# Kernel optimization log

Hardware: AMD Instinct MI355X
Metric: run time of the kernel (lower is better)

Reference implementation:

```python
import jax, jax.numpy as jnp
import numpy as np

N = 100000       # nodes
E0 = 1600000     # edges without self loops
E = E0 + N       # with self loops appended (attr 0), matching add_self_loops
DIN = 128        # input_dim
HID = 64         # nb_hidden_gnn (per-head out_channels)
HEADS = 4
EMB = 128
L = 3            # nb_layer
NEG_SLOPE = 0.2
BN_EPS = 1e-5


def setup_inputs() -> dict:
    key = jax.random.key(0)
    ks = jax.random.split(key, 12)
    # edges with no self loops; self loops (i,i) appended with edge_attr 0
    row = jax.random.randint(ks[0], (E0,), 0, N)
    off = jax.random.randint(ks[1], (E0,), 1, N)
    col = (row + off) % N
    loops = jnp.arange(N, dtype=row.dtype)
    edge_index = jnp.stack([jnp.concatenate([row, loops]),
                            jnp.concatenate([col, loops])])
    edge_attr = jnp.concatenate([jax.random.normal(ks[2], (E0, 1), jnp.float32),
                                 jnp.zeros((N, 1), jnp.float32)])
    x = jax.random.normal(ks[3], (N, DIN), jnp.float32)
    HC = HEADS * HID
    linN0 = jax.random.normal(ks[4], (DIN, HC)) * HC ** -0.5
    linN_rest = jax.random.normal(ks[5], (L - 1, HID, HC)) * HC ** -0.5
    linE_all = jax.random.normal(ks[6], (L, 1, HEADS)) * HEADS ** -0.5  # nb_edge_attr=1
    att_all = jax.random.normal(ks[7], (L, HEADS, 2 * HID + 1)) * (2 * HID + 1) ** -0.5
    bias_all = jnp.zeros((L, HID))  # concat=False -> bias [out_channels]
    bn_gamma = jnp.ones((L - 1, HID))
    bn_beta = jnp.zeros((L - 1, HID))
    W = jax.random.normal(ks[8], (HID, EMB)) * HID ** -0.5
    b = jnp.zeros((EMB,))
    return {"x": x, "edge_index": edge_index, "edge_attr": edge_attr,
            "linN0": linN0, "linN_rest": linN_rest, "linE_all": linE_all,
            "att_all": att_all, "bias_all": bias_all,
            "bn_gamma": bn_gamma, "bn_beta": bn_beta, "W": W, "b": b}


def _gcn_layer(x, row, col, edge_attr, linN, linE, att, bias, bn):
    n = x.shape[0]
    if bn is not None:
        gamma, beta = bn
        mu = x.mean(axis=0)
        var = x.var(axis=0)
        x = (x - mu) * jax.lax.rsqrt(var + BN_EPS) * gamma + beta
    h = (x @ linN).reshape(n, HEADS, HID)                 # [N,H,C]
    e = (edge_attr @ linE)                                # [E,H] (nb_edge_attr=1)
    att_i = att[:, :HID]                                  # [H,C]
    att_j = att[:, HID:2 * HID]                           # [H,C]
    att_e = att[:, 2 * HID:]                              # [H,1]
    # per-node partial scores avoid gathering full features twice
    s_i = jnp.einsum('nhc,hc->nh', h, att_i)
    s_j = jnp.einsum('nhc,hc->nh', h, att_j)
    logits = s_i[row] + s_j[col] + e * att_e[:, 0]        # [E,H]
    logits = jax.nn.leaky_relu(logits, NEG_SLOPE)
    # segment softmax over destination nodes (edge_index[1])
    m = jax.ops.segment_max(logits, col, num_segments=n)
    p = jnp.exp(logits - m[col])
    denom = jax.ops.segment_sum(p, col, num_segments=n)
    alpha = p / (denom[col] + 1e-16)
    # message: alpha * x[source], scatter-add to destination
    msg = alpha[:, :, None] * h[row]                      # [E,H,C]
    out = jax.ops.segment_sum(msg, col, num_segments=n)   # [N,H,C]
    out = out.mean(axis=1) + bias + h.mean(axis=1)        # concat=False, res=True
    return jax.nn.relu(out)


def reference(x, edge_index, edge_attr, linN0, linN_rest, linE_all, att_all,
              bias_all, bn_gamma, bn_beta, W, b):
    row, col = edge_index[0], edge_index[1]
    emb = x
    for l in range(L):
        linN = linN0 if l == 0 else linN_rest[l - 1]
        bn = None if l == 0 else (bn_gamma[l - 1], bn_beta[l - 1])
        emb = _gcn_layer(emb, row, col, edge_attr, linN, linE_all[l],
                         att_all[l], bias_all[l], bn)
    return emb @ W + b
```

## Files before the change

kernel.cpp:

```cpp
#include <hip/hip_runtime.h>
#include <math.h>

#define NN 100000
#define E0E 1600000
#define EE (E0E + NN)
#define NEG 0.2f
#define BNEPS 1e-5f
#define LOG2E 1.4426950408889634f

typedef float f4 __attribute__((ext_vector_type(4)));
typedef float f2 __attribute__((ext_vector_type(2)));
typedef short s8v __attribute__((ext_vector_type(8)));

__device__ __forceinline__ float wred_max(float v) {
#pragma unroll
  for (int m = 1; m < 64; m <<= 1) v = fmaxf(v, __shfl_xor(v, m, 64));
  return v;
}
__device__ __forceinline__ float wred_sum(float v) {
#pragma unroll
  for (int m = 1; m < 64; m <<= 1) v += __shfl_xor(v, m, 64);
  return v;
}
__device__ __forceinline__ float sel4(float a0, float a1, float a2, float a3, int hd) {
  return (hd & 2) ? ((hd & 1) ? a3 : a2) : ((hd & 1) ? a1 : a0);
}
__device__ __forceinline__ unsigned short f2bf(float x) {
  unsigned u = __float_as_uint(x);
  return (unsigned short)((u + 0x7fffu + ((u >> 16) & 1u)) >> 16);
}
__device__ __forceinline__ float bf2f(unsigned short s) {
  return __uint_as_float(((unsigned)s) << 16);
}

__global__ void k_zero_i32(int* p, int n) {
  int i = blockIdx.x * blockDim.x + threadIdx.x;
  if (i < n) p[i] = 0;
}
__global__ void k_zero_f64(double* p, int n) {
  int i = blockIdx.x * blockDim.x + threadIdx.x;
  if (i < n) p[i] = 0.0;
}
__global__ void k_count(const int* __restrict__ col, int* cnt, int e) {
  int i = blockIdx.x * blockDim.x + threadIdx.x;
  if (i < e) atomicAdd(&cnt[col[i]], 1);
}
#define SCAN_T 1024
__global__ void k_scan1(const int* __restrict__ cnt, int* partial, int n, int chunk) {
  int i = blockIdx.x * blockDim.x + threadIdx.x;
  int beg = i * chunk, end = min(n, beg + chunk);
  int s = 0;
  for (int j = beg; j < end; ++j) s += cnt[j];
  partial[i] = s;
}
__global__ void k_scan2(int* partial) {
  __shared__ int lds[SCAN_T];
  int t = threadIdx.x;
  int v = partial[t];
  lds[t] = v;
  __syncthreads();
  for (int off = 1; off < SCAN_T; off <<= 1) {
    int add = (t >= off) ? lds[t - off] : 0;
    __syncthreads();
    lds[t] += add;
    __syncthreads();
  }
  partial[t] = lds[t] - v;
}
__global__ void k_scan3(const int* __restrict__ cnt, const int* __restrict__ partial,
                        int* rowptr, int* cursor, int n, int chunk, int etot) {
  int i = blockIdx.x * blockDim.x + threadIdx.x;
  int beg = i * chunk, end = min(n, beg + chunk);
  int run = partial[i];
  for (int j = beg; j < end; ++j) {
    rowptr[j] = run;
    cursor[j] = run;
    run += cnt[j];
  }
  if (i == SCAN_T - 1) rowptr[n] = etot;
}
__global__ void k_scatter(const int* __restrict__ row, const int* __restrict__ col,
                          const float* __restrict__ ea, int* cursor, int2* csr, int e) {
  int i = blockIdx.x * blockDim.x + threadIdx.x;
  if (i < e) {
    int c = col[i];
    int p = atomicAdd(&cursor[c], 1);
    csr[p] = make_int2(row[i], __float_as_int(ea[i]));
  }
}

__global__ void k_bnstats(const float* __restrict__ x, double* sums, int n) {
  int f = threadIdx.x & 63;
  int rt = (blockIdx.x * blockDim.x + threadIdx.x) >> 6;
  int rstride = (gridDim.x * blockDim.x) >> 6;
  double s = 0.0, q = 0.0;
  for (int r = rt; r < n; r += rstride) {
    double v = (double)x[(size_t)r * 64 + f];
    s += v;
    q += v * v;
  }
  __shared__ double ls[256], lq[256];
  ls[threadIdx.x] = s;
  lq[threadIdx.x] = q;
  __syncthreads();
  if (threadIdx.x < 64) {
    s = ls[threadIdx.x] + ls[threadIdx.x + 64] + ls[threadIdx.x + 128] + ls[threadIdx.x + 192];
    q = lq[threadIdx.x] + lq[threadIdx.x + 64] + lq[threadIdx.x + 128] + lq[threadIdx.x + 192];
    atomicAdd(&sums[f], s);
    atomicAdd(&sums[64 + f], q);
  }
}
__global__ void k_bnfinal(const double* __restrict__ sums, const float* __restrict__ gamma,
                          const float* __restrict__ beta, float* AB, int n) {
  int f = threadIdx.x;
  if (f < 64) {
    double mean = sums[f] / n;
    double var = sums[64 + f] / n - mean * mean;
    float A = gamma[f] * rsqrtf((float)var + BNEPS);
    AB[f] = A;
    AB[64 + f] = beta[f] - (float)mean * A;
  }
}

__global__ void k_prepw(const float* __restrict__ W, const float* __restrict__ AB,
                        const float* __restrict__ bin, unsigned short* __restrict__ Wt,
                        float* __restrict__ cvec, int K, int N, int mode) {
  int n = threadIdx.x;
  if (n >= N) return;
  float c = (mode == 2) ? bin[n] : 0.f;
  for (int k = 0; k < K; ++k) {
    float w = W[k * N + n];
    float a = 1.f, b = 0.f;
    if (mode == 1) { a = AB[k]; b = AB[64 + k]; }
    Wt[n * K + k] = f2bf(a * w);
    c = fmaf(b, w, c);
  }
  cvec[n] = c;
}

template <int K, int CT, bool ATT, bool OB>
__global__ __launch_bounds__(256, 2) void k_gemm(const float* __restrict__ x,
                                                 const unsigned short* __restrict__ Wt,
                                                 const float* __restrict__ cvec,
                                                 const float* __restrict__ att,
                                                 void* __restrict__ houtv,
                                                 float* __restrict__ s_i,
                                                 float* __restrict__ s_j, int n,
                                                 int ntiles) {
  constexpr int KS = K / 32;
  constexpr int ROWB = 2 * K;
  constexpr int CPR = K / 8;
  constexpr int NCOL = 4 * CT * 16;
  __shared__ unsigned char xs[64 * ROWB];
  const int lane = threadIdx.x & 63;
  const int wv = threadIdx.x >> 6;
  const int l15 = lane & 15;
  const int lq = lane >> 4;
  const int colbase = wv * CT * 16;

  s8v wfr[CT][KS];
#pragma unroll
  for (int ct = 0; ct < CT; ++ct)
#pragma unroll
    for (int ks = 0; ks < KS; ++ks)
      wfr[ct][ks] = *(const s8v*)&Wt[(size_t)(colbase + ct * 16 + l15) * K + ks * 32 + lq * 8];
  float cb[CT][4];
#pragma unroll
  for (int ct = 0; ct < CT; ++ct)
#pragma unroll
    for (int r = 0; r < 4; ++r) cb[ct][r] = cvec[colbase + ct * 16 + lq * 4 + r];
  float ati[ATT ? CT : 1][4], atj[ATT ? CT : 1][4];
  if constexpr (ATT) {
    const float* ar = att + wv * 129;
#pragma unroll
    for (int ct = 0; ct < CT; ++ct)
#pragma unroll
      for (int r = 0; r < 4; ++r) {
        int cc = ct * 16 + lq * 4 + r;
        ati[ct][r] = ar[cc];
        atj[ct][r] = ar[64 + cc];
      }
  }

  for (int t = blockIdx.x; t < ntiles; t += gridDim.x) {
    const int row0 = t * 64;
    __syncthreads();
#pragma unroll
    for (int i = 0; i < (64 * CPR) / 256; ++i) {
      int c = threadIdx.x + i * 256;
      int row = c / CPR, kc = c % CPR;
      int rg = min(row0 + row, n - 1);
      const float* xp = x + (size_t)rg * K + kc * 8;
      f4 a0 = *(const f4*)xp;
      f4 a1 = *(const f4*)(xp + 4);
      union { s8v v; unsigned short u[8]; } pk;
      pk.u[0] = f2bf(a0[0]); pk.u[1] = f2bf(a0[1]); pk.u[2] = f2bf(a0[2]); pk.u[3] = f2bf(a0[3]);
      pk.u[4] = f2bf(a1[0]); pk.u[5] = f2bf(a1[1]); pk.u[6] = f2bf(a1[2]); pk.u[7] = f2bf(a1[3]);
      *(s8v*)&xs[row * ROWB + ((kc * 16) ^ ((row & 7) << 4))] = pk.v;
    }
    __syncthreads();
    f4 acc[4][CT];
#pragma unroll
    for (int rt = 0; rt < 4; ++rt)
#pragma unroll
      for (int ct = 0; ct < CT; ++ct) acc[rt][ct] = (f4)0.f;
#pragma unroll
    for (int ks = 0; ks < KS; ++ks) {
      s8v xf[4];
#pragma unroll
      for (int rt = 0; rt < 4; ++rt) {
        int row = rt * 16 + l15;
        int kb = ks * 64 + lq * 16;
        xf[rt] = *(const s8v*)&xs[row * ROWB + (kb ^ ((row & 7) << 4))];
      }
#pragma unroll
      for (int rt = 0; rt < 4; ++rt)
#pragma unroll
        for (int ct = 0; ct < CT; ++ct)
          acc[rt][ct] = __builtin_amdgcn_mfma_f32_16x16x32_bf16(wfr[ct][ks], xf[rt],
                                                                acc[rt][ct], 0, 0, 0);
    }
#pragma unroll
    for (int rt = 0; rt < 4; ++rt) {
      if (row0 + rt * 16 >= n) continue;
      const size_t xrow = (size_t)(row0 + rt * 16 + l15);
      float v[CT][4];
#pragma unroll
      for (int ct = 0; ct < CT; ++ct)
#pragma unroll
        for (int r = 0; r < 4; ++r) v[ct][r] = acc[rt][ct][r] + cb[ct][r];
      if constexpr (OB) {
        float* outp = (float*)houtv;
#pragma unroll
        for (int ct = 0; ct < CT; ++ct) {
          f4 o;
          o[0] = v[ct][0]; o[1] = v[ct][1]; o[2] = v[ct][2]; o[3] = v[ct][3];
          *(f4*)&outp[xrow * NCOL + colbase + ct * 16 + lq * 4] = o;
        }
      } else {
        unsigned short* hout = (unsigned short*)houtv;
#pragma unroll
        for (int ct = 0; ct < CT; ++ct) {
          ushort4 hb4;
          hb4.x = f2bf(v[ct][0]); hb4.y = f2bf(v[ct][1]);
          hb4.z = f2bf(v[ct][2]); hb4.w = f2bf(v[ct][3]);
          *(ushort4*)&hout[xrow * NCOL + colbase + ct * 16 + lq * 4] = hb4;
        }
      }
      if constexpr (ATT) {
        float pi = 0.f, pj = 0.f;
#pragma unroll
        for (int ct = 0; ct < CT; ++ct)
#pragma unroll
          for (int r = 0; r < 4; ++r) {
            pi = fmaf(v[ct][r], ati[ct][r], pi);
            pj = fmaf(v[ct][r], atj[ct][r], pj);
          }
        pi += __shfl_xor(pi, 16, 64); pi += __shfl_xor(pi, 32, 64);
        pj += __shfl_xor(pj, 16, 64); pj += __shfl_xor(pj, 32, 64);
        if (lane < 16) {
          s_i[xrow * 4 + wv] = pi;
          s_j[xrow * 4 + wv] = pj;
        }
      }
    }
  }
}

__global__ __launch_bounds__(256) void k_edge(const int* __restrict__ rowptr,
                                              const int2* __restrict__ csr,
                                              const float* __restrict__ s_i,
                                              const float* __restrict__ s_j,
                                              const unsigned short* __restrict__ hb,
                                              const float* __restrict__ linE,
                                              const float* __restrict__ att,
                                              const float* __restrict__ bias,
                                              float* __restrict__ xout, int n) {
  __shared__ float lp[4][64][4];
  __shared__ int lsrc[4][64];
  const int lane = threadIdx.x & 63;
  const int wid = threadIdx.x >> 6;
  int v = blockIdx.x * 4 + wid;
  if (v >= n) return;
  v = __builtin_amdgcn_readfirstlane(v);
  const int base = rowptr[v];
  const int deg = rowptr[v + 1] - base;

  const float coef0 = linE[0] * att[0 * 129 + 128];
  const float coef1 = linE[1] * att[1 * 129 + 128];
  const float coef2 = linE[2] * att[2 * 129 + 128];
  const float coef3 = linE[3] * att[3 * 129 + 128];
  const float sj0 = s_j[(size_t)v * 4 + 0];
  const float sj1 = s_j[(size_t)v * 4 + 1];
  const float sj2 = s_j[(size_t)v * 4 + 2];
  const float sj3 = s_j[(size_t)v * 4 + 3];

  auto edge_logits = [&](int i, int& src, float& g0, float& g1, float& g2, float& g3) {
    int2 pk = csr[i];
    src = pk.x;
    float ea = __int_as_float(pk.y);
    f4 siv = *(const f4*)&s_i[(size_t)src * 4];
    g0 = siv[0] + sj0 + ea * coef0; g0 = fmaxf(g0, g0 * NEG);
    g1 = siv[1] + sj1 + ea * coef1; g1 = fmaxf(g1, g1 * NEG);
    g2 = siv[2] + sj2 + ea * coef2; g2 = fmaxf(g2, g2 * NEG);
    g3 = siv[3] + sj3 + ea * coef3; g3 = fmaxf(g3, g3 * NEG);
  };

  const int hd = lane >> 4;
  float msel, rdsel;
  bool fast = (deg <= 64);
  if (fast) {
    float g0 = -INFINITY, g1 = -INFINITY, g2 = -INFINITY, g3 = -INFINITY;
    int src = 0;
    bool valid = lane < deg;
    if (valid) edge_logits(base + lane, src, g0, g1, g2, g3);
    float m0 = wred_max(g0), m1 = wred_max(g1), m2 = wred_max(g2), m3 = wred_max(g3);
    float p0 = valid ? exp2f((g0 - m0) * LOG2E) : 0.f;
    float p1 = valid ? exp2f((g1 - m1) * LOG2E) : 0.f;
    float p2 = valid ? exp2f((g2 - m2) * LOG2E) : 0.f;
    float p3 = valid ? exp2f((g3 - m3) * LOG2E) : 0.f;
    if (valid) {
      f4 pp; pp[0] = p0; pp[1] = p1; pp[2] = p2; pp[3] = p3;
      *(f4*)&lp[wid][lane][0] = pp;
      lsrc[wid][lane] = src;
    }
    float d0 = wred_sum(p0), d1 = wred_sum(p1), d2 = wred_sum(p2), d3 = wred_sum(p3);
    rdsel = 1.f / (sel4(d0, d1, d2, d3, hd) + 1e-16f);
    msel = 0.f;
  } else {
    float m0 = -INFINITY, m1 = -INFINITY, m2 = -INFINITY, m3 = -INFINITY;
    for (int c0 = 0; c0 < deg; c0 += 64) {
      int i = c0 + lane;
      if (i < deg) {
        int src; float g0, g1, g2, g3;
        edge_logits(base + i, src, g0, g1, g2, g3);
        m0 = fmaxf(m0, g0); m1 = fmaxf(m1, g1); m2 = fmaxf(m2, g2); m3 = fmaxf(m3, g3);
      }
    }
    m0 = wred_max(m0); m1 = wred_max(m1); m2 = wred_max(m2); m3 = wred_max(m3);
    float d0 = 0, d1 = 0, d2 = 0, d3 = 0;
    for (int c0 = 0; c0 < deg; c0 += 64) {
      int i = c0 + lane;
      if (i < deg) {
        int src; float g0, g1, g2, g3;
        edge_logits(base + i, src, g0, g1, g2, g3);
        d0 += exp2f((g0 - m0) * LOG2E);
        d1 += exp2f((g1 - m1) * LOG2E);
        d2 += exp2f((g2 - m2) * LOG2E);
        d3 += exp2f((g3 - m3) * LOG2E);
      }
    }
    d0 = wred_sum(d0); d1 = wred_sum(d1); d2 = wred_sum(d2); d3 = wred_sum(d3);
    msel = sel4(m0, m1, m2, m3, hd);
    rdsel = 1.f / (sel4(d0, d1, d2, d3, hd) + 1e-16f);
  }

  f4 acc;
  {
    ushort4 hr = *(const ushort4*)&hb[(size_t)v * 256 + lane * 4];
    acc[0] = bf2f(hr.x); acc[1] = bf2f(hr.y); acc[2] = bf2f(hr.z); acc[3] = bf2f(hr.w);
  }
  if (fast) {
    for (int e = 0; e < deg; ++e) {
      int src = lsrc[wid][e];
      float a = lp[wid][e][hd] * rdsel;
      ushort4 hr = *(const ushort4*)&hb[(size_t)src * 256 + lane * 4];
      acc[0] = fmaf(a, bf2f(hr.x), acc[0]);
      acc[1] = fmaf(a, bf2f(hr.y), acc[1]);
      acc[2] = fmaf(a, bf2f(hr.z), acc[2]);
      acc[3] = fmaf(a, bf2f(hr.w), acc[3]);
    }
  } else {
    const float sjsel = sel4(sj0, sj1, sj2, sj3, hd);
    const float cfsel = sel4(coef0, coef1, coef2, coef3, hd);
    for (int e = base; e < base + deg; ++e) {
      int2 pk = csr[e];
      int src = pk.x;
      float ea = __int_as_float(pk.y);
      f4 siv = *(const f4*)&s_i[(size_t)src * 4];
      float lg = sel4(siv[0], siv[1], siv[2], siv[3], hd) + sjsel + ea * cfsel;
      lg = fmaxf(lg, lg * NEG);
      float a = exp2f((lg - msel) * LOG2E) * rdsel;
      ushort4 hr = *(const ushort4*)&hb[(size_t)src * 256 + lane * 4];
      acc[0] = fmaf(a, bf2f(hr.x), acc[0]);
      acc[1] = fmaf(a, bf2f(hr.y), acc[1]);
      acc[2] = fmaf(a, bf2f(hr.z), acc[2]);
      acc[3] = fmaf(a, bf2f(hr.w), acc[3]);
    }
  }
#pragma unroll
  for (int m = 16; m < 64; m <<= 1) {
    acc[0] += __shfl_xor(acc[0], m, 64);
    acc[1] += __shfl_xor(acc[1], m, 64);
    acc[2] += __shfl_xor(acc[2], m, 64);
    acc[3] += __shfl_xor(acc[3], m, 64);
  }
  if (lane < 16) {
    f4 bv = *(const f4*)&bias[lane * 4];
    f4 o;
#pragma unroll
    for (int c = 0; c < 4; ++c) o[c] = fmaxf(acc[c] * 0.25f + bv[c], 0.f);
    *(f4*)&xout[(size_t)v * 64 + lane * 4] = o;
  }
}

extern "C" void kernel_launch(void* const* d_in, const int* in_sizes, int n_in,
                              void* d_out, int out_size, void* d_ws, size_t ws_size,
                              hipStream_t stream) {
  const float* x_in = (const float*)d_in[0];
  const int* ei = (const int*)d_in[1];
  const float* eattr = (const float*)d_in[2];
  const float* linN0 = (const float*)d_in[3];
  const float* linNr = (const float*)d_in[4];
  const float* linE = (const float*)d_in[5];
  const float* attA = (const float*)d_in[6];
  const float* biasA = (const float*)d_in[7];
  const float* bng = (const float*)d_in[8];
  const float* bnb = (const float*)d_in[9];
  const float* W = (const float*)d_in[10];
  const float* bb = (const float*)d_in[11];
  float* out = (float*)d_out;

  const int* row = ei;
  const int* col = ei + EE;

  char* ws = (char*)d_ws;
  size_t o = 0;
  auto alloc = [&](size_t bytes) {
    void* p = ws + o;
    o += (bytes + 255) & ~(size_t)255;
    return p;
  };
  int* cnt = (int*)alloc((size_t)NN * 4);
  int* cursor = (int*)alloc((size_t)NN * 4);
  int* rowptr = (int*)alloc((size_t)(NN + 1) * 4);
  int* partial = (int*)alloc((size_t)SCAN_T * 4);
  int2* csr = (int2*)alloc((size_t)EE * 8);
  unsigned short* h = (unsigned short*)alloc((size_t)NN * 256 * 2);
  float* si = (float*)alloc((size_t)NN * 4 * 4);
  float* sj = (float*)alloc((size_t)NN * 4 * 4);
  float* xa = (float*)alloc((size_t)NN * 64 * 4);
  float* xb = (float*)alloc((size_t)NN * 64 * 4);
  double* bnsum = (double*)alloc(256 * 8);
  float* AB = (float*)alloc(128 * 4);
  unsigned short* Wt = (unsigned short*)alloc((size_t)256 * 128 * 2);
  float* cvec = (float*)alloc(256 * 4);
  if (o > ws_size) return;

  const int chunk = (NN + SCAN_T - 1) / SCAN_T;
  const int NTILES = (NN + 63) / 64;
  const int GG = 521;

  k_zero_i32<<<(NN + 255) / 256, 256, 0, stream>>>(cnt, NN);
  k_zero_f64<<<1, 256, 0, stream>>>(bnsum, 256);
  k_count<<<(EE + 255) / 256, 256, 0, stream>>>(col, cnt, EE);
  k_scan1<<<4, 256, 0, stream>>>(cnt, partial, NN, chunk);
  k_scan2<<<1, SCAN_T, 0, stream>>>(partial);
  k_scan3<<<4, 256, 0, stream>>>(cnt, partial, rowptr, cursor, NN, chunk, EE);
  k_scatter<<<(EE + 255) / 256, 256, 0, stream>>>(row, col, eattr, cursor, csr, EE);

  k_prepw<<<1, 256, 0, stream>>>(linN0, nullptr, nullptr, Wt, cvec, 128, 256, 0);
  k_gemm<128, 4, true, false><<<GG, 256, 0, stream>>>(x_in, Wt, cvec, attA + 0, h, si, sj,
                                                      NN, NTILES);
  k_edge<<<NN / 4, 256, 0, stream>>>(rowptr, csr, si, sj, h, linE + 0, attA + 0, biasA + 0, xa, NN);

  k_bnstats<<<256, 256, 0, stream>>>(xa, bnsum, NN);
  k_bnfinal<<<1, 64, 0, stream>>>(bnsum, bng + 0, bnb + 0, AB, NN);
  k_prepw<<<1, 256, 0, stream>>>(linNr, AB, nullptr, Wt, cvec, 64, 256, 1);
  k_gemm<64, 4, true, false><<<GG, 256, 0, stream>>>(xa, Wt, cvec, attA + 516, h, si, sj,
                                                     NN, NTILES);
  k_edge<<<NN / 4, 256, 0, stream>>>(rowptr, csr, si, sj, h, linE + 4, attA + 516, biasA + 64, xb, NN);

  k_bnstats<<<256, 256, 0, stream>>>(xb, bnsum + 128, NN);
  k_bnfinal<<<1, 64, 0, stream>>>(bnsum + 128, bng + 64, bnb + 64, AB, NN);
  k_prepw<<<1, 256, 0, stream>>>(linNr + 64 * 256, AB, nullptr, Wt, cvec, 64, 256, 1);
  k_gemm<64, 4, true, false><<<GG, 256, 0, stream>>>(xb, Wt, cvec, attA + 2 * 516, h, si, sj,
                                                     NN, NTILES);
  k_edge<<<NN / 4, 256, 0, stream>>>(rowptr, csr, si, sj, h, linE + 8, attA + 2 * 516, biasA + 128, xa, NN);

  k_prepw<<<1, 256, 0, stream>>>(W, nullptr, bb, Wt, cvec, 64, 128, 2);
  k_gemm<64, 2, false, true><<<GG, 256, 0, stream>>>(xa, Wt, cvec, nullptr, out, nullptr,
                                                     nullptr, NN, NTILES);
}
```

Before: 940.1 us.

## Fuse batchnorm statistics into edge kernel and persistent-loop edge aggregation

The edge-aggregation kernel becomes a grid-stride persistent loop over nodes. It accumulates per-feature sums and sums of squares of its output, then reduces them per block and adds them atomically into the batchnorm buffer. This removes the separate stats pass that re-read the activations, and the finalize step moves into the weight-prep kernel. The zeroing kernels are merged into one, the fast-path gather is unrolled by four for more loads in flight, and the gemm grid now uses one block per tile instead of a fixed count. Statistics are now accumulated in float per thread before the double atomics, which slightly changes precision.

```diff
diff --git a/kernel.cpp b/kernel.cpp
--- a/kernel.cpp
+++ b/kernel.cpp
@@ -33,13 +33,10 @@
   return __uint_as_float(((unsigned)s) << 16);
 }
 
-__global__ void k_zero_i32(int* p, int n) {
+__global__ void k_init(int* cnt, double* bnsum, int n) {
   int i = blockIdx.x * blockDim.x + threadIdx.x;
-  if (i < n) p[i] = 0;
-}
-__global__ void k_zero_f64(double* p, int n) {
-  int i = blockIdx.x * blockDim.x + threadIdx.x;
-  if (i < n) p[i] = 0.0;
+  if (i < n) cnt[i] = 0;
+  if (i < 256) bnsum[i] = 0.0;
 }
 __global__ void k_count(const int* __restrict__ col, int* cnt, int e) {
   int i = blockIdx.x * blockDim.x + threadIdx.x;
@@ -89,53 +86,32 @@
   }
 }
 
-__global__ void k_bnstats(const float* __restrict__ x, double* sums, int n) {
-  int f = threadIdx.x & 63;
-  int rt = (blockIdx.x * blockDim.x + threadIdx.x) >> 6;
-  int rstride = (gridDim.x * blockDim.x) >> 6;
-  double s = 0.0, q = 0.0;
-  for (int r = rt; r < n; r += rstride) {
-    double v = (double)x[(size_t)r * 64 + f];
-    s += v;
-    q += v * v;
-  }
-  __shared__ double ls[256], lq[256];
-  ls[threadIdx.x] = s;
-  lq[threadIdx.x] = q;
-  __syncthreads();
-  if (threadIdx.x < 64) {
-    s = ls[threadIdx.x] + ls[threadIdx.x + 64] + ls[threadIdx.x + 128] + ls[threadIdx.x + 192];
-    q = lq[threadIdx.x] + lq[threadIdx.x + 64] + lq[threadIdx.x + 128] + lq[threadIdx.x + 192];
-    atomicAdd(&sums[f], s);
-    atomicAdd(&sums[64 + f], q);
-  }
-}
-__global__ void k_bnfinal(const double* __restrict__ sums, const float* __restrict__ gamma,
-                          const float* __restrict__ beta, float* AB, int n) {
-  int f = threadIdx.x;
-  if (f < 64) {
-    double mean = sums[f] / n;
-    double var = sums[64 + f] / n - mean * mean;
-    float A = gamma[f] * rsqrtf((float)var + BNEPS);
-    AB[f] = A;
-    AB[64 + f] = beta[f] - (float)mean * A;
-  }
-}
-
-__global__ void k_prepw(const float* __restrict__ W, const float* __restrict__ AB,
+__global__ void k_prepw(const float* __restrict__ W, const double* __restrict__ bnsum,
+                        const float* __restrict__ gamma, const float* __restrict__ beta,
                         const float* __restrict__ bin, unsigned short* __restrict__ Wt,
                         float* __restrict__ cvec, int K, int N, int mode) {
-  int n = threadIdx.x;
-  if (n >= N) return;
-  float c = (mode == 2) ? bin[n] : 0.f;
+  __shared__ float ABl[128];
+  int t = threadIdx.x;
+  if (mode == 1) {
+    if (t < 64) {
+      double mean = bnsum[t] / NN;
+      double var = bnsum[64 + t] / NN - mean * mean;
+      float A = gamma[t] * rsqrtf((float)var + BNEPS);
+      ABl[t] = A;
+      ABl[64 + t] = beta[t] - (float)mean * A;
+    }
+    __syncthreads();
+  }
+  if (t >= N) return;
+  float c = (mode == 2) ? bin[t] : 0.f;
   for (int k = 0; k < K; ++k) {
-    float w = W[k * N + n];
+    float w = W[k * N + t];
     float a = 1.f, b = 0.f;
-    if (mode == 1) { a = AB[k]; b = AB[64 + k]; }
-    Wt[n * K + k] = f2bf(a * w);
+    if (mode == 1) { a = ABl[k]; b = ABl[64 + k]; }
+    Wt[t * K + k] = f2bf(a * w);
     c = fmaf(b, w, c);
   }
-  cvec[n] = c;
+  cvec[t] = c;
 }
 
 template <int K, int CT, bool ATT, bool OB>
@@ -267,6 +243,7 @@
   }
 }
 
+template <bool BNS>
 __global__ __launch_bounds__(256) void k_edge(const int* __restrict__ rowptr,
                                               const int2* __restrict__ csr,
                                               const float* __restrict__ s_i,
@@ -275,132 +252,184 @@
                                               const float* __restrict__ linE,
                                               const float* __restrict__ att,
                                               const float* __restrict__ bias,
-                                              float* __restrict__ xout, int n) {
+                                              float* __restrict__ xout,
+                                              double* __restrict__ bnsum, int n) {
   __shared__ float lp[4][64][4];
   __shared__ int lsrc[4][64];
+  __shared__ float bS[4][64], bQ[4][64];
   const int lane = threadIdx.x & 63;
   const int wid = threadIdx.x >> 6;
-  int v = blockIdx.x * 4 + wid;
-  if (v >= n) return;
-  v = __builtin_amdgcn_readfirstlane(v);
-  const int base = rowptr[v];
-  const int deg = rowptr[v + 1] - base;
+  const int hd = lane >> 4;
 
   const float coef0 = linE[0] * att[0 * 129 + 128];
   const float coef1 = linE[1] * att[1 * 129 + 128];
   const float coef2 = linE[2] * att[2 * 129 + 128];
   const float coef3 = linE[3] * att[3 * 129 + 128];
-  const float sj0 = s_j[(size_t)v * 4 + 0];
-  const float sj1 = s_j[(size_t)v * 4 + 1];
-  const float sj2 = s_j[(size_t)v * 4 + 2];
-  const float sj3 = s_j[(size_t)v * 4 + 3];
-
-  auto edge_logits = [&](int i, int& src, float& g0, float& g1, float& g2, float& g3) {
-    int2 pk = csr[i];
-    src = pk.x;
-    float ea = __int_as_float(pk.y);
-    f4 siv = *(const f4*)&s_i[(size_t)src * 4];
-    g0 = siv[0] + sj0 + ea * coef0; g0 = fmaxf(g0, g0 * NEG);
-    g1 = siv[1] + sj1 + ea * coef1; g1 = fmaxf(g1, g1 * NEG);
-    g2 = siv[2] + sj2 + ea * coef2; g2 = fmaxf(g2, g2 * NEG);
-    g3 = siv[3] + sj3 + ea * coef3; g3 = fmaxf(g3, g3 * NEG);
-  };
-
-  const int hd = lane >> 4;
-  float msel, rdsel;
-  bool fast = (deg <= 64);
-  if (fast) {
-    float g0 = -INFINITY, g1 = -INFINITY, g2 = -INFINITY, g3 = -INFINITY;
-    int src = 0;
-    bool valid = lane < deg;
-    if (valid) edge_logits(base + lane, src, g0, g1, g2, g3);
-    float m0 = wred_max(g0), m1 = wred_max(g1), m2 = wred_max(g2), m3 = wred_max(g3);
-    float p0 = valid ? exp2f((g0 - m0) * LOG2E) : 0.f;
-    float p1 = valid ? exp2f((g1 - m1) * LOG2E) : 0.f;
-    float p2 = valid ? exp2f((g2 - m2) * LOG2E) : 0.f;
-    float p3 = valid ? exp2f((g3 - m3) * LOG2E) : 0.f;
-    if (valid) {
-      f4 pp; pp[0] = p0; pp[1] = p1; pp[2] = p2; pp[3] = p3;
-      *(f4*)&lp[wid][lane][0] = pp;
-      lsrc[wid][lane] = src;
-    }
-    float d0 = wred_sum(p0), d1 = wred_sum(p1), d2 = wred_sum(p2), d3 = wred_sum(p3);
-    rdsel = 1.f / (sel4(d0, d1, d2, d3, hd) + 1e-16f);
-    msel = 0.f;
-  } else {
-    float m0 = -INFINITY, m1 = -INFINITY, m2 = -INFINITY, m3 = -INFINITY;
-    for (int c0 = 0; c0 < deg; c0 += 64) {
-      int i = c0 + lane;
-      if (i < deg) {
-        int src; float g0, g1, g2, g3;
-        edge_logits(base + i, src, g0, g1, g2, g3);
-        m0 = fmaxf(m0, g0); m1 = fmaxf(m1, g1); m2 = fmaxf(m2, g2); m3 = fmaxf(m3, g3);
-      }
-    }
-    m0 = wred_max(m0); m1 = wred_max(m1); m2 = wred_max(m2); m3 = wred_max(m3);
-    float d0 = 0, d1 = 0, d2 = 0, d3 = 0;
-    for (int c0 = 0; c0 < deg; c0 += 64) {
-      int i = c0 + lane;
-      if (i < deg) {
-        int src; float g0, g1, g2, g3;
-        edge_logits(base + i, src, g0, g1, g2, g3);
-        d0 += exp2f((g0 - m0) * LOG2E);
-        d1 += exp2f((g1 - m1) * LOG2E);
-        d2 += exp2f((g2 - m2) * LOG2E);
-        d3 += exp2f((g3 - m3) * LOG2E);
-      }
-    }
-    d0 = wred_sum(d0); d1 = wred_sum(d1); d2 = wred_sum(d2); d3 = wred_sum(d3);
-    msel = sel4(m0, m1, m2, m3, hd);
-    rdsel = 1.f / (sel4(d0, d1, d2, d3, hd) + 1e-16f);
-  }
-
-  f4 acc;
-  {
-    ushort4 hr = *(const ushort4*)&hb[(size_t)v * 256 + lane * 4];
-    acc[0] = bf2f(hr.x); acc[1] = bf2f(hr.y); acc[2] = bf2f(hr.z); acc[3] = bf2f(hr.w);
-  }
-  if (fast) {
-    for (int e = 0; e < deg; ++e) {
-      int src = lsrc[wid][e];
-      float a = lp[wid][e][hd] * rdsel;
-      ushort4 hr = *(const ushort4*)&hb[(size_t)src * 256 + lane * 4];
-      acc[0] = fmaf(a, bf2f(hr.x), acc[0]);
-      acc[1] = fmaf(a, bf2f(hr.y), acc[1]);
-      acc[2] = fmaf(a, bf2f(hr.z), acc[2]);
-      acc[3] = fmaf(a, bf2f(hr.w), acc[3]);
-    }
-  } else {
-    const float sjsel = sel4(sj0, sj1, sj2, sj3, hd);
-    const float cfsel = sel4(coef0, coef1, coef2, coef3, hd);
-    for (int e = base; e < base + deg; ++e) {
-      int2 pk = csr[e];
-      int src = pk.x;
+  float accS[4] = {0.f, 0.f, 0.f, 0.f}, accQ[4] = {0.f, 0.f, 0.f, 0.f};
+
+  for (int v0 = blockIdx.x * 4 + wid; v0 < n; v0 += gridDim.x * 4) {
+    const int v = __builtin_amdgcn_readfirstlane(v0);
+    const int base = rowptr[v];
+    const int deg = rowptr[v + 1] - base;
+    const float sj0 = s_j[(size_t)v * 4 + 0];
+    const float sj1 = s_j[(size_t)v * 4 + 1];
+    const float sj2 = s_j[(size_t)v * 4 + 2];
+    const float sj3 = s_j[(size_t)v * 4 + 3];
+
+    f4 accI;
+    {
+      ushort4 hr = *(const ushort4*)&hb[(size_t)v * 256 + lane * 4];
+      accI[0] = bf2f(hr.x); accI[1] = bf2f(hr.y); accI[2] = bf2f(hr.z); accI[3] = bf2f(hr.w);
+    }
+
+    auto edge_logits = [&](int i, int& src, float& g0, float& g1, float& g2, float& g3) {
+      int2 pk = csr[i];
+      src = pk.x;
       float ea = __int_as_float(pk.y);
       f4 siv = *(const f4*)&s_i[(size_t)src * 4];
-      float lg = sel4(siv[0], siv[1], siv[2], siv[3], hd) + sjsel + ea * cfsel;
-      lg = fmaxf(lg, lg * NEG);
-      float a = exp2f((lg - msel) * LOG2E) * rdsel;
-      ushort4 hr = *(const ushort4*)&hb[(size_t)src * 256 + lane * 4];
-      acc[0] = fmaf(a, bf2f(hr.x), acc[0]);
-      acc[1] = fmaf(a, bf2f(hr.y), acc[1]);
-      acc[2] = fmaf(a, bf2f(hr.z), acc[2]);
-      acc[3] = fmaf(a, bf2f(hr.w), acc[3]);
-    }
-  }
-#pragma unroll
-  for (int m = 16; m < 64; m <<= 1) {
-    acc[0] += __shfl_xor(acc[0], m, 64);
-    acc[1] += __shfl_xor(acc[1], m, 64);
-    acc[2] += __shfl_xor(acc[2], m, 64);
-    acc[3] += __shfl_xor(acc[3], m, 64);
-  }
-  if (lane < 16) {
-    f4 bv = *(const f4*)&bias[lane * 4];
-    f4 o;
-#pragma unroll
-    for (int c = 0; c < 4; ++c) o[c] = fmaxf(acc[c] * 0.25f + bv[c], 0.f);
-    *(f4*)&xout[(size_t)v * 64 + lane * 4] = o;
+      g0 = siv[0] + sj0 + ea * coef0; g0 = fmaxf(g0, g0 * NEG);
+      g1 = siv[1] + sj1 + ea * coef1; g1 = fmaxf(g1, g1 * NEG);
+      g2 = siv[2] + sj2 + ea * coef2; g2 = fmaxf(g2, g2 * NEG);
+      g3 = siv[3] + sj3 + ea * coef3; g3 = fmaxf(g3, g3 * NEG);
+    };
+
+    float rdsel;
+    f4 accE = {0.f, 0.f, 0.f, 0.f};
+    bool fast = (deg <= 64);
+    if (fast) {
+      float g0 = -INFINITY, g1 = -INFINITY, g2 = -INFINITY, g3 = -INFINITY;
+      int src = 0;
+      bool valid = lane < deg;
+      if (valid) edge_logits(base + lane, src, g0, g1, g2, g3);
+      float m0 = wred_max(g0), m1 = wred_max(g1), m2 = wred_max(g2), m3 = wred_max(g3);
+      float p0 = valid ? exp2f((g0 - m0) * LOG2E) : 0.f;
+      float p1 = valid ? exp2f((g1 - m1) * LOG2E) : 0.f;
+      float p2 = valid ? exp2f((g2 - m2) * LOG2E) : 0.f;
+      float p3 = valid ? exp2f((g3 - m3) * LOG2E) : 0.f;
+      if (valid) {
+        f4 pp; pp[0] = p0; pp[1] = p1; pp[2] = p2; pp[3] = p3;
+        *(f4*)&lp[wid][lane][0] = pp;
+        lsrc[wid][lane] = src;
+      }
+      float d0 = wred_sum(p0), d1 = wred_sum(p1), d2 = wred_sum(p2), d3 = wred_sum(p3);
+      rdsel = 1.f / (sel4(d0, d1, d2, d3, hd) + 1e-16f);
+      int e = 0;
+      for (; e + 4 <= deg; e += 4) {
+        int s0 = lsrc[wid][e + 0], s1 = lsrc[wid][e + 1];
+        int s2 = lsrc[wid][e + 2], s3 = lsrc[wid][e + 3];
+        float a0 = lp[wid][e + 0][hd], a1 = lp[wid][e + 1][hd];
+        float a2 = lp[wid][e + 2][hd], a3 = lp[wid][e + 3][hd];
+        ushort4 h0 = *(const ushort4*)&hb[(size_t)s0 * 256 + lane * 4];
+        ushort4 h1 = *(const ushort4*)&hb[(size_t)s1 * 256 + lane * 4];
+        ushort4 h2 = *(const ushort4*)&hb[(size_t)s2 * 256 + lane * 4];
+        ushort4 h3 = *(const ushort4*)&hb[(size_t)s3 * 256 + lane * 4];
+        accE[0] = fmaf(a0, bf2f(h0.x), accE[0]); accE[1] = fmaf(a0, bf2f(h0.y), accE[1]);
+        accE[2] = fmaf(a0, bf2f(h0.z), accE[2]); accE[3] = fmaf(a0, bf2f(h0.w), accE[3]);
+        accE[0] = fmaf(a1, bf2f(h1.x), accE[0]); accE[1] = fmaf(a1, bf2f(h1.y), accE[1]);
+        accE[2] = fmaf(a1, bf2f(h1.z), accE[2]); accE[3] = fmaf(a1, bf2f(h1.w), accE[3]);
+        accE[0] = fmaf(a2, bf2f(h2.x), accE[0]); accE[1] = fmaf(a2, bf2f(h2.y), accE[1]);
+        accE[2] = fmaf(a2, bf2f(h2.z), accE[2]); accE[3] = fmaf(a2, bf2f(h2.w), accE[3]);
+        accE[0] = fmaf(a3, bf2f(h3.x), accE[0]); accE[1] = fmaf(a3, bf2f(h3.y), accE[1]);
+        accE[2] = fmaf(a3, bf2f(h3.z), accE[2]); accE[3] = fmaf(a3, bf2f(h3.w), accE[3]);
+      }
+      for (; e < deg; ++e) {
+        int s0 = lsrc[wid][e];
+        float a0 = lp[wid][e][hd];
+        ushort4 h0 = *(const ushort4*)&hb[(size_t)s0 * 256 + lane * 4];
+        accE[0] = fmaf(a0, bf2f(h0.x), accE[0]); accE[1] = fmaf(a0, bf2f(h0.y), accE[1]);
+        accE[2] = fmaf(a0, bf2f(h0.z), accE[2]); accE[3] = fmaf(a0, bf2f(h0.w), accE[3]);
+      }
+    } else {
+      float m0 = -INFINITY, m1 = -INFINITY, m2 = -INFINITY, m3 = -INFINITY;
+      for (int c0 = 0; c0 < deg; c0 += 64) {
+        int i = c0 + lane;
+        if (i < deg) {
+          int src; float g0, g1, g2, g3;
+          edge_logits(base + i, src, g0, g1, g2, g3);
+          m0 = fmaxf(m0, g0); m1 = fmaxf(m1, g1); m2 = fmaxf(m2, g2); m3 = fmaxf(m3, g3);
+        }
+      }
+      m0 = wred_max(m0); m1 = wred_max(m1); m2 = wred_max(m2); m3 = wred_max(m3);
+      float d0 = 0, d1 = 0, d2 = 0, d3 = 0;
+      for (int c0 = 0; c0 < deg; c0 += 64) {
+        int i = c0 + lane;
+        if (i < deg) {
+          int src; float g0, g1, g2, g3;
+          edge_logits(base + i, src, g0, g1, g2, g3);
+          d0 += exp2f((g0 - m0) * LOG2E);
+          d1 += exp2f((g1 - m1) * LOG2E);
+          d2 += exp2f((g2 - m2) * LOG2E);
+          d3 += exp2f((g3 - m3) * LOG2E);
+        }
+      }
+      d0 = wred_sum(d0); d1 = wred_sum(d1); d2 = wred_sum(d2); d3 = wred_sum(d3);
+      float msel = sel4(m0, m1, m2, m3, hd);
+      rdsel = 1.f / (sel4(d0, d1, d2, d3, hd) + 1e-16f);
+      const float sjsel = sel4(sj0, sj1, sj2, sj3, hd);
+      const float cfsel = sel4(coef0, coef1, coef2, coef3, hd);
+      for (int e = base; e < base + deg; ++e) {
+        int2 pk = csr[e];
+        int src = pk.x;
+        float ea = __int_as_float(pk.y);
+        f4 siv = *(const f4*)&s_i[(size_t)src * 4];
+        float lg = sel4(siv[0], siv[1], siv[2], siv[3], hd) + sjsel + ea * cfsel;
+        lg = fmaxf(lg, lg * NEG);
+        float a = exp2f((lg - msel) * LOG2E);
+        ushort4 hr = *(const ushort4*)&hb[(size_t)src * 256 + lane * 4];
+        accE[0] = fmaf(a, bf2f(hr.x), accE[0]);
+        accE[1] = fmaf(a, bf2f(hr.y), accE[1]);
+        accE[2] = fmaf(a, bf2f(hr.z), accE[2]);
+        accE[3] = fmaf(a, bf2f(hr.w), accE[3]);
+      }
+    }
+    f4 acc;
+#pragma unroll
+    for (int c = 0; c < 4; ++c) acc[c] = fmaf(rdsel, accE[c], accI[c]);
+#pragma unroll
+    for (int m = 16; m < 64; m <<= 1) {
+      acc[0] += __shfl_xor(acc[0], m, 64);
+      acc[1] += __shfl_xor(acc[1], m, 64);
+      acc[2] += __shfl_xor(acc[2], m, 64);
+      acc[3] += __shfl_xor(acc[3], m, 64);
+    }
+    if (lane < 16) {
+      f4 bv = *(const f4*)&bias[lane * 4];
+      f4 o;
+#pragma unroll
+      for (int c = 0; c < 4; ++c) o[c] = fmaxf(acc[c] * 0.25f + bv[c], 0.f);
+      *(f4*)&xout[(size_t)v * 64 + lane * 4] = o;
+      if constexpr (BNS) {
+#pragma unroll
+        for (int c = 0; c < 4; ++c) {
+          accS[c] += o[c];
+          accQ[c] += o[c] * o[c];
+        }
+      }
+    }
+  }
+
+  if constexpr (BNS) {
+    if (lane < 16) {
+#pragma unroll
+      for (int c = 0; c < 4; ++c) {
+        bS[wid][lane * 4 + c] = accS[c];
+        bQ[wid][lane * 4 + c] = accQ[c];
+      }
+    }
+    __syncthreads();
+    int t = threadIdx.x;
+    if (t < 64) {
+      float s = 0.f;
+#pragma unroll
+      for (int w = 0; w < 4; ++w) s += bS[w][t];
+      atomicAdd(&bnsum[t], (double)s);
+    } else if (t < 128) {
+      int f = t - 64;
+      float q = 0.f;
+#pragma unroll
+      for (int w = 0; w < 4; ++w) q += bQ[w][f];
+      atomicAdd(&bnsum[64 + f], (double)q);
+    }
   }
 }
 
@@ -442,43 +471,41 @@
   float* xa = (float*)alloc((size_t)NN * 64 * 4);
   float* xb = (float*)alloc((size_t)NN * 64 * 4);
   double* bnsum = (double*)alloc(256 * 8);
-  float* AB = (float*)alloc(128 * 4);
   unsigned short* Wt = (unsigned short*)alloc((size_t)256 * 128 * 2);
   float* cvec = (float*)alloc(256 * 4);
   if (o > ws_size) return;
 
   const int chunk = (NN + SCAN_T - 1) / SCAN_T;
   const int NTILES = (NN + 63) / 64;
-  const int GG = 521;
-
-  k_zero_i32<<<(NN + 255) / 256, 256, 0, stream>>>(cnt, NN);
-  k_zero_f64<<<1, 256, 0, stream>>>(bnsum, 256);
+  const int EG = 2048;
+
+  k_init<<<(NN + 255) / 256, 256, 0, stream>>>(cnt, bnsum, NN);
   k_count<<<(EE + 255) / 256, 256, 0, stream>>>(col, cnt, EE);
   k_scan1<<<4, 256, 0, stream>>>(cnt, partial, NN, chunk);
   k_scan2<<<1, SCAN_T, 0, stream>>>(partial);
   k_scan3<<<4, 256, 0, stream>>>(cnt, partial, rowptr, cursor, NN, chunk, EE);
   k_scatter<<<(EE + 255) / 256, 256, 0, stream>>>(row, col, eattr, cursor, csr, EE);
 
-  k_prepw<<<1, 256, 0, stream>>>(linN0, nullptr, nullptr, Wt, cvec, 128, 256, 0);
-  k_gemm<128, 4, true, false><<<GG, 256, 0, stream>>>(x_in, Wt, cvec, attA + 0, h, si, sj,
-                                                      NN, NTILES);
-  k_edge<<<NN / 4, 256, 0, stream>>>(rowptr, csr, si, sj, h, linE + 0, attA + 0, biasA + 0, xa, NN);
-
-  k_bnstats<<<256, 256, 0, stream>>>(xa, bnsum, NN);
-  k_bnfinal<<<1, 64, 0, stream>>>(bnsum, bng + 0, bnb + 0, AB, NN);
-  k_prepw<<<1, 256, 0, stream>>>(linNr, AB, nullptr, Wt, cvec, 64, 256, 1);
-  k_gemm<64, 4, true, false><<<GG, 256, 0, stream>>>(xa, Wt, cvec, attA + 516, h, si, sj,
-                                                     NN, NTILES);
-  k_edge<<<NN / 4, 256, 0, stream>>>(rowptr, csr, si, sj, h, linE + 4, attA + 516, biasA + 64, xb, NN);
-
-  k_bnstats<<<256, 256, 0, stream>>>(xb, bnsum + 128, NN);
-  k_bnfinal<<<1, 64, 0, stream>>>(bnsum + 128, bng + 64, bnb + 64, AB, NN);
-  k_prepw<<<1, 256, 0, stream>>>(linNr + 64 * 256, AB, nullptr, Wt, cvec, 64, 256, 1);
-  k_gemm<64, 4, true, false><<<GG, 256, 0, stream>>>(xb, Wt, cvec, attA + 2 * 516, h, si, sj,
-                                                     NN, NTILES);
-  k_edge<<<NN / 4, 256, 0, stream>>>(rowptr, csr, si, sj, h, linE + 8, attA + 2 * 516, biasA + 128, xa, NN);
-
-  k_prepw<<<1, 256, 0, stream>>>(W, nullptr, bb, Wt, cvec, 64, 128, 2);
-  k_gemm<64, 2, false, true><<<GG, 256, 0, stream>>>(xa, Wt, cvec, nullptr, out, nullptr,
-                                                     nullptr, NN, NTILES);
-}
+  k_prepw<<<1, 256, 0, stream>>>(linN0, nullptr, nullptr, nullptr, nullptr, Wt, cvec, 128, 256, 0);
+  k_gemm<128, 4, true, false><<<NTILES, 256, 0, stream>>>(x_in, Wt, cvec, attA + 0, h, si, sj,
+                                                          NN, NTILES);
+  k_edge<true><<<EG, 256, 0, stream>>>(rowptr, csr, si, sj, h, linE + 0, attA + 0, biasA + 0,
+                                       xa, bnsum, NN);
+
+  k_prepw<<<1, 256, 0, stream>>>(linNr, bnsum, bng, bnb, nullptr, Wt, cvec, 64, 256, 1);
+  k_gemm<64, 4, true, false><<<NTILES, 256, 0, stream>>>(xa, Wt, cvec, attA + 516, h, si, sj,
+                                                         NN, NTILES);
+  k_edge<true><<<EG, 256, 0, stream>>>(rowptr, csr, si, sj, h, linE + 4, attA + 516, biasA + 64,
+                                       xb, bnsum + 128, NN);
+
+  k_prepw<<<1, 256, 0, stream>>>(linNr + 64 * 256, bnsum + 128, bng + 64, bnb + 64, nullptr,
+                                 Wt, cvec, 64, 256, 1);
+  k_gemm<64, 4, true, false><<<NTILES, 256, 0, stream>>>(xb, Wt, cvec, attA + 2 * 516, h, si, sj,
+                                                         NN, NTILES);
+  k_edge<false><<<EG, 256, 0, stream>>>(rowptr, csr, si, sj, h, linE + 8, attA + 2 * 516,
+                                        biasA + 128, xa, nullptr, NN);
+
+  k_prepw<<<1, 256, 0, stream>>>(W, nullptr, nullptr, nullptr, bb, Wt, cvec, 64, 128, 2);
+  k_gemm<64, 2, false, true><<<NTILES, 256, 0, stream>>>(xa, Wt, cvec, nullptr, out, nullptr,
+                                                         nullptr, NN, NTILES);
+}
```

Measured after the change: 974.3 us. 3.6% more time.
